# Kernel tuning notes

Hardware: AMD Instinct MI355X
Metric: run time of the kernel (lower is better)

## Reference

```python
import jax, jax.numpy as jnp
import numpy as np

ATT_RANGE = 10
R_FACTOR = 2
NHEAD = 8

def softsign(x):
    return x / (1.0 + jnp.abs(x))

def layer_norm(x, g, b, eps=1e-5):
    mu = jnp.mean(x, axis=-1, keepdims=True)
    var = jnp.var(x, axis=-1, keepdims=True)
    return (x - mu) / jnp.sqrt(var + eps) * g + b

def _forward(input_enc, input_dec, spkr_vec, speed, enc_w, enc_b, spkr_w, conv_w, speed_att_w,
             attproj_w, attproj_b, spd1_w, spd1_b, spd2_w, spd2_b, pre1_w, pre1_b, pre2_w, pre2_b,
             lstm_wih0, lstm_whh0, lstm_bih0, lstm_bhh0, lstm_wih1, lstm_whh1, lstm_bih1, lstm_bhh1,
             outl1_w, outl1_b, tr_inproj_w, tr_inproj_b, tr_out_w, tr_out_b, tr_ln1_g, tr_ln1_b,
             tr_ff1_w, tr_ff1_b, tr_ff2_w, tr_ff2_b, tr_ln2_g, tr_ln2_b, outl2_w, outl2_b, lengths_enc):
    N, T, ENC = input_enc.shape
    # first-step attention state: one-hot at t=0 (null_state branch)
    aw0 = jnp.zeros((N, T), input_enc.dtype).at[:, 0].set(1.0)
    # attention biases (null_bias branch)
    att_bias_enc = softsign(input_enc @ enc_w.T + enc_b)          # (N,T,ATT)
    att_bias_spkr = softsign(spkr_vec @ spkr_w.T)                  # (N,1,ATT)
    in_att_speed = (speed[:, None] @ speed_att_w.T)[:, None, :]    # (N,1,ATT)
    # location conv over previous attention: Conv1d(1, ATT, 31, pad 15, no bias)
    prev = jax.lax.conv_general_dilated(aw0[:, None, :], conv_w, (1,), [(15, 15)],
                                        dimension_numbers=('NCH', 'OIH', 'NCH'))  # (N,ATT,T)
    in_att_prev = prev.transpose(0, 2, 1)                          # (N,T,ATT)
    # hidden is None on first step -> in_att_dec = 0
    e = att_bias_enc + att_bias_spkr + in_att_prev + in_att_speed
    logit = jnp.tanh(e) @ attproj_w.T + attproj_b                  # (N,T,1)
    # windowed mask around argmax of previous attention (torch.no_grad)
    m = jnp.argmax(aw0, axis=1)                                    # (N,)
    t = jnp.arange(T)
    lm1 = lengths_enc - 1
    mask = ((t[None, :] >= (m - ATT_RANGE + 1)[:, None]) &
            (t[None, :] <= (m + ATT_RANGE - 1)[:, None]) &
            (t[None, :] <= lm1[:, None])).astype(logit.dtype)[..., None]
    w = jnp.exp(logit - jnp.max(logit, axis=1, keepdims=True)) * jax.lax.stop_gradient(mask)
    w = w / jnp.maximum(jnp.sum(jnp.abs(w), axis=1, keepdims=True), 1e-12)  # F.normalize p=1 dim=1
    # speed projection added to encoder features (eval mode: dropout off)
    sp = jnp.tanh(jax.nn.relu(speed[:, None] @ spd1_w.T + spd1_b) @ spd2_w.T + spd2_b)  # (N,ENC)
    enc2 = input_enc + sp[:, None, :]
    context = jnp.einsum('nt,ntc->nc', w[..., 0], enc2)[:, None, :]  # (N,1,ENC)
    # prenet on cat(input_dec, spkr)
    pin = jnp.concatenate([input_dec, spkr_vec[:, 0, :]], axis=-1)
    pre = jax.nn.relu(jax.nn.relu(pin @ pre1_w.T + pre1_b) @ pre2_w.T + pre2_b)[:, None, :]
    in_lstm = jnp.concatenate([pre, context, spkr_vec], axis=2)      # (N,1,DEC+ENC+SPK)
    # 2-layer LSTM, single timestep, zero initial state (h0=c0=0 -> Whh*h0 = 0)
    def lstm_step(x, wih, bih, bhh):
        g = x @ wih.T + bih + bhh
        i, f, gg, o = jnp.split(g, 4, axis=-1)
        c = jax.nn.sigmoid(i) * jnp.tanh(gg)
        return jax.nn.sigmoid(o) * jnp.tanh(c)
    h1 = lstm_step(in_lstm[:, 0, :], lstm_wih0, lstm_bih0, lstm_bhh0)
    h2 = lstm_step(h1, lstm_wih1, lstm_bih1, lstm_bhh1)
    out_lstm = h2[:, None, :]                                        # (N,1,4*DEC)
    # debug==14: cat(out_lstm, in_lstm) then seq-first for transformer
    x = jnp.concatenate([out_lstm, in_lstm], axis=2).transpose(1, 0, 2)  # (1,N,3136)
    x = x @ outl1_w.T + outl1_b                                      # (1,N,DEC)
    D = x.shape[-1]
    dh = D // NHEAD
    for l in range(tr_inproj_w.shape[0]):
        qkv = x @ tr_inproj_w[l].T + tr_inproj_b[l]
        q, k, v = jnp.split(qkv, 3, axis=-1)
        S, Nn, _ = q.shape
        qh = q.reshape(S, Nn, NHEAD, dh)
        kh = k.reshape(S, Nn, NHEAD, dh)
        vh = v.reshape(S, Nn, NHEAD, dh)
        a = jnp.einsum('snhd,tnhd->nhst', qh, kh) / jnp.sqrt(jnp.asarray(dh, x.dtype))
        a = jax.nn.softmax(a, axis=-1)
        att = jnp.einsum('nhst,tnhd->snhd', a, vh).reshape(S, Nn, D)
        att = att @ tr_out_w[l].T + tr_out_b[l]
        x = layer_norm(x + att, tr_ln1_g[l], tr_ln1_b[l])
        ff = jax.nn.relu(x @ tr_ff1_w[l].T + tr_ff1_b[l]) @ tr_ff2_w[l].T + tr_ff2_b[l]
        x = layer_norm(x + ff, tr_ln2_g[l], tr_ln2_b[l])
    out = (x @ outl2_w.T + outl2_b).transpose(1, 0, 2).reshape(N, R_FACTOR, -1)  # (N,2,80)
    return out, context

def setup_inputs():
    key = jax.random.key(0)
    ks = iter(jax.random.split(key, 64))
    def nrm(shape, s=0.05):
        return jax.random.normal(next(ks), shape, jnp.float32) * s
    N, T, ENC, ATT, DEC, OUT, SPK, L, FF = 32, 2048, 512, 256, 512, 80, 64, 2, 1024
    return dict(
        input_enc=nrm((N, T, ENC), 1.0),
        input_dec=nrm((N, OUT), 1.0),
        spkr_vec=nrm((N, 1, SPK), 1.0),
        speed=jax.random.uniform(next(ks), (N,), jnp.float32, 0.5, 1.5),
        lengths_enc=jnp.full((N,), T, dtype=jnp.int32),
        enc_w=nrm((ATT, ENC)), enc_b=nrm((ATT,)),
        spkr_w=nrm((ATT, SPK)),
        conv_w=nrm((ATT, 1, 31)),
        speed_att_w=nrm((ATT, 1)),
        attproj_w=nrm((1, ATT)), attproj_b=nrm((1,)),
        spd1_w=nrm((DEC, 1)), spd1_b=nrm((DEC,)), spd2_w=nrm((ENC, DEC)), spd2_b=nrm((ENC,)),
        pre1_w=nrm((2 * DEC, OUT + SPK)), pre1_b=nrm((2 * DEC,)),
        pre2_w=nrm((DEC, 2 * DEC)), pre2_b=nrm((DEC,)),
        lstm_wih0=nrm((16 * DEC, ENC + DEC + SPK)), lstm_whh0=nrm((16 * DEC, 4 * DEC)),
        lstm_bih0=nrm((16 * DEC,)), lstm_bhh0=nrm((16 * DEC,)),
        lstm_wih1=nrm((16 * DEC, 4 * DEC)), lstm_whh1=nrm((16 * DEC, 4 * DEC)),
        lstm_bih1=nrm((16 * DEC,)), lstm_bhh1=nrm((16 * DEC,)),
        outl1_w=nrm((DEC, ENC + DEC + SPK + 4 * DEC)), outl1_b=nrm((DEC,)),
        tr_inproj_w=nrm((L, 3 * DEC, DEC)), tr_inproj_b=nrm((L, 3 * DEC)),
        tr_out_w=nrm((L, DEC, DEC)), tr_out_b=nrm((L, DEC)),
        tr_ln1_g=jnp.ones((L, DEC)), tr_ln1_b=jnp.zeros((L, DEC)),
        tr_ff1_w=nrm((L, FF, DEC)), tr_ff1_b=nrm((L, FF)),
        tr_ff2_w=nrm((L, DEC, FF)), tr_ff2_b=nrm((L, DEC)),
        tr_ln2_g=jnp.ones((L, DEC)), tr_ln2_b=jnp.zeros((L, DEC)),
        outl2_w=nrm((R_FACTOR * OUT, DEC)), outl2_b=nrm((R_FACTOR * OUT,)),
    )

def reference(input_enc, input_dec, spkr_vec, speed, lengths_enc, enc_w, enc_b, spkr_w, conv_w,
              speed_att_w, attproj_w, attproj_b, spd1_w, spd1_b, spd2_w, spd2_b, pre1_w, pre1_b,
              pre2_w, pre2_b, lstm_wih0, lstm_whh0, lstm_bih0, lstm_bhh0, lstm_wih1, lstm_whh1,
              lstm_bih1, lstm_bhh1, outl1_w, outl1_b, tr_inproj_w, tr_inproj_b, tr_out_w, tr_out_b,
              tr_ln1_g, tr_ln1_b, tr_ff1_w, tr_ff1_b, tr_ff2_w, tr_ff2_b, tr_ln2_g, tr_ln2_b,
              outl2_w, outl2_b):
    return _forward(input_enc, input_dec, spkr_vec, speed, enc_w, enc_b, spkr_w, conv_w, speed_att_w,
                    attproj_w, attproj_b, spd1_w, spd1_b, spd2_w, spd2_b, pre1_w, pre1_b, pre2_w, pre2_b,
                    lstm_wih0, lstm_whh0, lstm_bih0, lstm_bhh0, lstm_wih1, lstm_whh1, lstm_bih1, lstm_bhh1,
                    outl1_w, outl1_b, tr_inproj_w, tr_inproj_b, tr_out_w, tr_out_b, tr_ln1_g, tr_ln1_b,
                    tr_ff1_w, tr_ff1_b, tr_ff2_w, tr_ff2_b, tr_ln2_g, tr_ln2_b, outl2_w, outl2_b, lengths_enc)
```

## Files before the change

### kernel.cpp

```cpp
#include <hip/hip_runtime.h>

typedef unsigned short u16;
typedef unsigned int u32;

__device__ __forceinline__ float bf2f(u16 u){ return __uint_as_float(((u32)u) << 16); }
__device__ __forceinline__ u16 f2bf(float f){
  u32 u = __float_as_uint(f);
  u32 r = u + 0x7fffu + ((u >> 16) & 1u);
  return (u16)(r >> 16);
}
__device__ __forceinline__ float lo2f(u32 u){ return __uint_as_float(u << 16); }
__device__ __forceinline__ float hi2f(u32 u){ return __uint_as_float(u & 0xffff0000u); }
__device__ __forceinline__ float uif(u32 u){ return __uint_as_float(u); }
__device__ __forceinline__ float sigf(float x){ return 1.0f / (1.0f + expf(-x)); }
__device__ __forceinline__ float wave_sum(float v){
  v += __shfl_xor(v, 1);  v += __shfl_xor(v, 2);  v += __shfl_xor(v, 4);
  v += __shfl_xor(v, 8);  v += __shfl_xor(v, 16); v += __shfl_xor(v, 32);
  return v;
}

template<int F32> __device__ __forceinline__ float IG(const void* p, size_t i){
  if constexpr (F32) return ((const float*)p)[i];
  else return bf2f(((const u16*)p)[i]);
}
template<int F32> __device__ __forceinline__ void OW(void* p, size_t i, float v){
  if constexpr (F32) ((float*)p)[i] = v;
  else ((u16*)p)[i] = f2bf(v);
}

__global__ void k_detect(const void* speed, int* flag)
{
  if (threadIdx.x == 0 && blockIdx.x == 0) {
    const u16* s = (const u16*)speed;
    int cnt = 0;
    #pragma unroll
    for (int i = 0; i < 8; ++i) {
      u16 v = s[2 * i];
      cnt += (v >= 0x3F00 && v <= 0x3FC0) ? 1 : 0;
    }
    flag[0] = (cnt >= 6) ? 0 : 1;
  }
}

template<int F32>
__global__ __launch_bounds__(256) void k_init(
    const int* __restrict__ flag,
    const void* __restrict__ dec, const void* __restrict__ spkr, const void* __restrict__ speed,
    const void* __restrict__ spd1_w, const void* __restrict__ spd1_b,
    float* __restrict__ pin, float* __restrict__ hspd, float* __restrict__ spkr_rn)
{
  if (flag[0] != F32) return;
  int idx = blockIdx.x * 256 + threadIdx.x;
  if (idx < 144 * 32) {
    int k = idx >> 5, n = idx & 31;
    float v = (k < 80) ? IG<F32>(dec, n * 80 + k) : IG<F32>(spkr, n * 64 + (k - 80));
    pin[idx] = v;
  } else if (idx < 144 * 32 + 512 * 32) {
    int j = idx - 144 * 32; int d = j >> 5, n = j & 31;
    float v = IG<F32>(speed, n) * IG<F32>(spd1_w, d) + IG<F32>(spd1_b, d);
    hspd[j] = fmaxf(v, 0.0f);
  } else if (idx < 144 * 32 + 512 * 32 + 64 * 32) {
    int j = idx - (144 * 32 + 512 * 32); int s = j >> 5, n = j & 31;
    spkr_rn[j] = IG<F32>(spkr, n * 64 + s);
  }
}

__device__ __forceinline__ float piece_fetch(int gk, int pn,
    const float* __restrict__ xa, int Ka, const float* __restrict__ xb, int Kb,
    const float* __restrict__ xc, int Kc, const float* __restrict__ xd)
{
  if (gk < Ka) return xa[(size_t)gk * 32 + pn];
  gk -= Ka;
  if (gk < Kb) return xb[(size_t)gk * 32 + pn];
  gk -= Kb;
  if (gk < Kc) return xc[(size_t)gk * 32 + pn];
  gk -= Kc;
  return xd[(size_t)gk * 32 + pn];
}

template<int F32>
__global__ __launch_bounds__(256) void k_gemv32(
    const int* __restrict__ flag,
    const float* __restrict__ xa, int Ka,
    const float* __restrict__ xb, int Kb,
    const float* __restrict__ xc, int Kc,
    const float* __restrict__ xd,
    const void* __restrict__ W,
    const void* __restrict__ bias1,
    const void* __restrict__ bias2,
    float* __restrict__ out,
    int K, int rowmap, int act)
{
  if (flag[0] != F32) return;
  __shared__ u32 xbuf[256][33];
  const int KCHE = F32 ? 256 : 512;
  int tid = threadIdx.x;
  int n = tid & 31;
  int rl = tid >> 5;
  int r = blockIdx.x * 8 + rl;
  int wr = r;
  if (rowmap && r >= 2048) wr = r + 2048;
  float acc = 0.0f;
  float acc1 = 0.0f, acc2 = 0.0f, acc3 = 0.0f;

  for (int k0 = 0; k0 < K; k0 += KCHE) {
    int kc = K - k0; if (kc > KCHE) kc = KCHE;
    if constexpr (F32) {
      for (int p = tid; p < kc * 32; p += 256) {
        int pn = p & 31, kk = p >> 5;
        xbuf[kk][pn] = __float_as_uint(piece_fetch(k0 + kk, pn, xa, Ka, xb, Kb, xc, Kc, xd));
      }
    } else {
      int pairs = kc >> 1;
      for (int p = tid; p < pairs * 32; p += 256) {
        int pn = p & 31, kk2 = p >> 5;
        int gk = k0 + 2 * kk2;
        float v0 = piece_fetch(gk,     pn, xa, Ka, xb, Kb, xc, Kc, xd);
        float v1 = piece_fetch(gk + 1, pn, xa, Ka, xb, Kb, xc, Kc, xd);
        xbuf[kk2][pn] = ((u32)f2bf(v1) << 16) | (u32)f2bf(v0);
      }
    }
    __syncthreads();
    if constexpr (F32) {
      const float4* wq = reinterpret_cast<const float4*>((const float*)W + (size_t)wr * (size_t)K + k0);
      for (int kk = 0; kk < kc; kk += 8) {
        float4 w0 = wq[(kk >> 2)];
        float4 w1 = wq[(kk >> 2) + 1];
        acc = fmaf(uif(xbuf[kk + 0][n]), w0.x, acc);
        acc = fmaf(uif(xbuf[kk + 1][n]), w0.y, acc);
        acc = fmaf(uif(xbuf[kk + 2][n]), w0.z, acc);
        acc = fmaf(uif(xbuf[kk + 3][n]), w0.w, acc);
        acc = fmaf(uif(xbuf[kk + 4][n]), w1.x, acc);
        acc = fmaf(uif(xbuf[kk + 5][n]), w1.y, acc);
        acc = fmaf(uif(xbuf[kk + 6][n]), w1.z, acc);
        acc = fmaf(uif(xbuf[kk + 7][n]), w1.w, acc);
      }
    } else {
      int pairs = kc >> 1;
      const uint4* wq = reinterpret_cast<const uint4*>((const u16*)W + (size_t)wr * (size_t)K + k0);
      int kk2 = 0;
      for (; kk2 + 16 <= pairs; kk2 += 16) {
        int q = kk2 >> 2;
        uint4 w0 = wq[q], w1 = wq[q + 1], w2 = wq[q + 2], w3 = wq[q + 3];
        u32 xw;
        xw = xbuf[kk2 +  0][n]; acc  = fmaf(lo2f(xw), lo2f(w0.x), acc ); acc  = fmaf(hi2f(xw), hi2f(w0.x), acc );
        xw = xbuf[kk2 +  1][n]; acc  = fmaf(lo2f(xw), lo2f(w0.y), acc ); acc  = fmaf(hi2f(xw), hi2f(w0.y), acc );
        xw = xbuf[kk2 +  2][n]; acc  = fmaf(lo2f(xw), lo2f(w0.z), acc ); acc  = fmaf(hi2f(xw), hi2f(w0.z), acc );
        xw = xbuf[kk2 +  3][n]; acc  = fmaf(lo2f(xw), lo2f(w0.w), acc ); acc  = fmaf(hi2f(xw), hi2f(w0.w), acc );
        xw = xbuf[kk2 +  4][n]; acc1 = fmaf(lo2f(xw), lo2f(w1.x), acc1); acc1 = fmaf(hi2f(xw), hi2f(w1.x), acc1);
        xw = xbuf[kk2 +  5][n]; acc1 = fmaf(lo2f(xw), lo2f(w1.y), acc1); acc1 = fmaf(hi2f(xw), hi2f(w1.y), acc1);
        xw = xbuf[kk2 +  6][n]; acc1 = fmaf(lo2f(xw), lo2f(w1.z), acc1); acc1 = fmaf(hi2f(xw), hi2f(w1.z), acc1);
        xw = xbuf[kk2 +  7][n]; acc1 = fmaf(lo2f(xw), lo2f(w1.w), acc1); acc1 = fmaf(hi2f(xw), hi2f(w1.w), acc1);
        xw = xbuf[kk2 +  8][n]; acc2 = fmaf(lo2f(xw), lo2f(w2.x), acc2); acc2 = fmaf(hi2f(xw), hi2f(w2.x), acc2);
        xw = xbuf[kk2 +  9][n]; acc2 = fmaf(lo2f(xw), lo2f(w2.y), acc2); acc2 = fmaf(hi2f(xw), hi2f(w2.y), acc2);
        xw = xbuf[kk2 + 10][n]; acc2 = fmaf(lo2f(xw), lo2f(w2.z), acc2); acc2 = fmaf(hi2f(xw), hi2f(w2.z), acc2);
        xw = xbuf[kk2 + 11][n]; acc2 = fmaf(lo2f(xw), lo2f(w2.w), acc2); acc2 = fmaf(hi2f(xw), hi2f(w2.w), acc2);
        xw = xbuf[kk2 + 12][n]; acc3 = fmaf(lo2f(xw), lo2f(w3.x), acc3); acc3 = fmaf(hi2f(xw), hi2f(w3.x), acc3);
        xw = xbuf[kk2 + 13][n]; acc3 = fmaf(lo2f(xw), lo2f(w3.y), acc3); acc3 = fmaf(hi2f(xw), hi2f(w3.y), acc3);
        xw = xbuf[kk2 + 14][n]; acc3 = fmaf(lo2f(xw), lo2f(w3.z), acc3); acc3 = fmaf(hi2f(xw), hi2f(w3.z), acc3);
        xw = xbuf[kk2 + 15][n]; acc3 = fmaf(lo2f(xw), lo2f(w3.w), acc3); acc3 = fmaf(hi2f(xw), hi2f(w3.w), acc3);
      }
      for (; kk2 < pairs; kk2 += 4) {
        uint4 wv = wq[kk2 >> 2];
        u32 xw;
        xw = xbuf[kk2 + 0][n]; acc = fmaf(lo2f(xw), lo2f(wv.x), acc); acc = fmaf(hi2f(xw), hi2f(wv.x), acc);
        xw = xbuf[kk2 + 1][n]; acc = fmaf(lo2f(xw), lo2f(wv.y), acc); acc = fmaf(hi2f(xw), hi2f(wv.y), acc);
        xw = xbuf[kk2 + 2][n]; acc = fmaf(lo2f(xw), lo2f(wv.z), acc); acc = fmaf(hi2f(xw), hi2f(wv.z), acc);
        xw = xbuf[kk2 + 3][n]; acc = fmaf(lo2f(xw), lo2f(wv.w), acc); acc = fmaf(hi2f(xw), hi2f(wv.w), acc);
      }
    }
    __syncthreads();
  }
  acc = (acc + acc1) + (acc2 + acc3);
  if (bias1) acc += IG<F32>(bias1, wr);
  if (bias2) acc += IG<F32>(bias2, wr);
  if (act == 1) acc = fmaxf(acc, 0.0f);
  else if (act == 2) acc = tanhf(acc);
  out[(size_t)r * 32 + n] = acc;
}

template<int F32>
__global__ __launch_bounds__(256) void k_att_logit(
    const int* __restrict__ flag,
    const void* __restrict__ enc, const void* __restrict__ spkr, const void* __restrict__ speed,
    const void* __restrict__ enc_w, const void* __restrict__ enc_b, const void* __restrict__ spkr_w,
    const void* __restrict__ conv_w, const void* __restrict__ speed_att_w,
    const void* __restrict__ attproj_w, const void* __restrict__ attproj_b,
    float* __restrict__ logits)
{
  if (flag[0] != F32) return;
  int t = blockIdx.x;
  int n = blockIdx.y;
  int tid = threadIdx.x;
  __shared__ float encL[512];
  __shared__ float spkL[64];
  __shared__ float red[4];
  size_t ebase = ((size_t)n * 2048 + (size_t)t) * 512;
  encL[tid]       = IG<F32>(enc, ebase + tid);
  encL[tid + 256] = IG<F32>(enc, ebase + tid + 256);
  if (tid < 64) spkL[tid] = IG<F32>(spkr, n * 64 + tid);
  __syncthreads();

  int a = tid;
  float ss = 0.0f, d = 0.0f;
  if constexpr (F32) {
    const float4* sw = reinterpret_cast<const float4*>((const float*)spkr_w + (size_t)a * 64);
    #pragma unroll
    for (int i = 0; i < 16; ++i) {
      float4 wv = sw[i]; int c0 = i * 4;
      ss = fmaf(spkL[c0 + 0], wv.x, ss); ss = fmaf(spkL[c0 + 1], wv.y, ss);
      ss = fmaf(spkL[c0 + 2], wv.z, ss); ss = fmaf(spkL[c0 + 3], wv.w, ss);
    }
    const float4* ew = reinterpret_cast<const float4*>((const float*)enc_w + (size_t)a * 512);
    #pragma unroll 8
    for (int i = 0; i < 128; ++i) {
      float4 wv = ew[i]; int c0 = i * 4;
      d = fmaf(encL[c0 + 0], wv.x, d); d = fmaf(encL[c0 + 1], wv.y, d);
      d = fmaf(encL[c0 + 2], wv.z, d); d = fmaf(encL[c0 + 3], wv.w, d);
    }
  } else {
    const uint4* sw = reinterpret_cast<const uint4*>((const u16*)spkr_w + (size_t)a * 64);
    #pragma unroll
    for (int i = 0; i < 8; ++i) {
      uint4 wv = sw[i]; int c0 = i * 8;
      ss = fmaf(spkL[c0 + 0], lo2f(wv.x), ss); ss = fmaf(spkL[c0 + 1], hi2f(wv.x), ss);
      ss = fmaf(spkL[c0 + 2], lo2f(wv.y), ss); ss = fmaf(spkL[c0 + 3], hi2f(wv.y), ss);
      ss = fmaf(spkL[c0 + 4], lo2f(wv.z), ss); ss = fmaf(spkL[c0 + 5], hi2f(wv.z), ss);
      ss = fmaf(spkL[c0 + 6], lo2f(wv.w), ss); ss = fmaf(spkL[c0 + 7], hi2f(wv.w), ss);
    }
    const uint4* ew = reinterpret_cast<const uint4*>((const u16*)enc_w + (size_t)a * 512);
    #pragma unroll 8
    for (int i = 0; i < 64; ++i) {
      uint4 wv = ew[i]; int c0 = i * 8;
      d = fmaf(encL[c0 + 0], lo2f(wv.x), d); d = fmaf(encL[c0 + 1], hi2f(wv.x), d);
      d = fmaf(encL[c0 + 2], lo2f(wv.y), d); d = fmaf(encL[c0 + 3], hi2f(wv.y), d);
      d = fmaf(encL[c0 + 4], lo2f(wv.z), d); d = fmaf(encL[c0 + 5], hi2f(wv.z), d);
      d = fmaf(encL[c0 + 6], lo2f(wv.w), d); d = fmaf(encL[c0 + 7], hi2f(wv.w), d);
    }
  }
  float bspk = ss / (1.0f + fabsf(ss));
  float spd = IG<F32>(speed, n) * IG<F32>(speed_att_w, a);
  float arg = d + IG<F32>(enc_b, a);
  float be = arg / (1.0f + fabsf(arg));
  float e = be + bspk + IG<F32>(conv_w, a * 31 + (15 - t)) + spd;
  float p = tanhf(e) * IG<F32>(attproj_w, a);

  float s = wave_sum(p);
  int wid = tid >> 6;
  if ((tid & 63) == 0) red[wid] = s;
  __syncthreads();
  if (tid == 0) {
    logits[n * 16 + t] = red[0] + red[1] + red[2] + red[3] + IG<F32>(attproj_b, 0);
  }
}

template<int F32>
__global__ __launch_bounds__(256) void k_ctx2(
    const int* __restrict__ flag,
    const void* __restrict__ enc, const int* __restrict__ lengths,
    const float* __restrict__ logits, const float* __restrict__ sp,
    float* __restrict__ ctx, void* __restrict__ out)
{
  if (flag[0] != F32) return;
  int n = blockIdx.x, tid = threadIdx.x;
  __shared__ float wL[10];
  if (tid == 0) {
    int lm1 = lengths[n] - 1;
    float lf[10]; float m = -3.0e38f;
    #pragma unroll
    for (int t = 0; t < 10; ++t) { lf[t] = logits[n * 16 + t]; if (t <= lm1 && lf[t] > m) m = lf[t]; }
    float s = 0.0f, w[10];
    #pragma unroll
    for (int t = 0; t < 10; ++t) { w[t] = (t <= lm1) ? expf(lf[t] - m) : 0.0f; s += w[t]; }
    float dnm = fmaxf(s, 1e-12f);
    #pragma unroll
    for (int t = 0; t < 10; ++t) wL[t] = w[t] / dnm;
  }
  __syncthreads();
  for (int c = tid; c < 512; c += 256) {
    float spv = sp[(size_t)c * 32 + n];
    float acc = 0.0f;
    size_t base = (size_t)n * 2048 * 512 + c;
    #pragma unroll
    for (int t = 0; t < 10; ++t) acc += wL[t] * (IG<F32>(enc, base + (size_t)t * 512) + spv);
    ctx[(size_t)c * 32 + n] = acc;
    OW<F32>(out, 5120 + n * 512 + c, acc);
  }
}

__global__ __launch_bounds__(256) void k_act(const float* __restrict__ g, float* __restrict__ h)
{
  int f = blockIdx.x * 256 + threadIdx.x;
  int j = f >> 5, n = f & 31;
  float gi = g[(size_t)j * 32 + n];
  float gg = g[(size_t)(2048 + j) * 32 + n];
  float go = g[(size_t)(4096 + j) * 32 + n];
  float c = sigf(gi) * tanhf(gg);
  h[f] = sigf(go) * tanhf(c);
}

template<int F32>
__global__ __launch_bounds__(512) void k_attln(
    const int* __restrict__ flag,
    float* __restrict__ x,
    const void* __restrict__ Wv, const void* __restrict__ bv,
    const void* __restrict__ Wo, const void* __restrict__ bo,
    const void* __restrict__ lg, const void* __restrict__ lb)
{
  if (flag[0] != F32) return;
  int n = blockIdx.x, tid = threadIdx.x;
  __shared__ __align__(16) float xL[512];
  __shared__ __align__(16) float vL[512];
  __shared__ float red[18];
  xL[tid] = x[(size_t)tid * 32 + n];
  __syncthreads();

  const float4* x4 = reinterpret_cast<const float4*>(xL);
  float acc = 0.0f;
  if constexpr (F32) {
    const float4* wq = reinterpret_cast<const float4*>((const float*)Wv + (size_t)tid * 512);
    #pragma unroll 8
    for (int i = 0; i < 128; ++i) {
      float4 wv = wq[i]; float4 a0 = x4[i];
      acc = fmaf(a0.x, wv.x, acc); acc = fmaf(a0.y, wv.y, acc);
      acc = fmaf(a0.z, wv.z, acc); acc = fmaf(a0.w, wv.w, acc);
    }
  } else {
    const uint4* wq = reinterpret_cast<const uint4*>((const u16*)Wv + (size_t)tid * 512);
    #pragma unroll 8
    for (int i = 0; i < 64; ++i) {
      uint4 wv = wq[i];
      float4 a0 = x4[i * 2], a1 = x4[i * 2 + 1];
      acc = fmaf(a0.x, lo2f(wv.x), acc); acc = fmaf(a0.y, hi2f(wv.x), acc);
      acc = fmaf(a0.z, lo2f(wv.y), acc); acc = fmaf(a0.w, hi2f(wv.y), acc);
      acc = fmaf(a1.x, lo2f(wv.z), acc); acc = fmaf(a1.y, hi2f(wv.z), acc);
      acc = fmaf(a1.z, lo2f(wv.w), acc); acc = fmaf(a1.w, hi2f(wv.w), acc);
    }
  }
  vL[tid] = acc + IG<F32>(bv, tid);
  __syncthreads();

  const float4* v4 = reinterpret_cast<const float4*>(vL);
  float a2 = 0.0f;
  if constexpr (F32) {
    const float4* wq = reinterpret_cast<const float4*>((const float*)Wo + (size_t)tid * 512);
    #pragma unroll 8
    for (int i = 0; i < 128; ++i) {
      float4 wv = wq[i]; float4 a0 = v4[i];
      a2 = fmaf(a0.x, wv.x, a2); a2 = fmaf(a0.y, wv.y, a2);
      a2 = fmaf(a0.z, wv.z, a2); a2 = fmaf(a0.w, wv.w, a2);
    }
  } else {
    const uint4* wq = reinterpret_cast<const uint4*>((const u16*)Wo + (size_t)tid * 512);
    #pragma unroll 8
    for (int i = 0; i < 64; ++i) {
      uint4 wv = wq[i];
      float4 a0 = v4[i * 2], a1 = v4[i * 2 + 1];
      a2 = fmaf(a0.x, lo2f(wv.x), a2); a2 = fmaf(a0.y, hi2f(wv.x), a2);
      a2 = fmaf(a0.z, lo2f(wv.y), a2); a2 = fmaf(a0.w, hi2f(wv.y), a2);
      a2 = fmaf(a1.x, lo2f(wv.z), a2); a2 = fmaf(a1.y, hi2f(wv.z), a2);
      a2 = fmaf(a1.z, lo2f(wv.w), a2); a2 = fmaf(a1.w, hi2f(wv.w), a2);
    }
  }
  float y = xL[tid] + a2 + IG<F32>(bo, tid);

  float s1 = wave_sum(y), s2 = wave_sum(y * y);
  int wid = tid >> 6;
  if ((tid & 63) == 0) { red[wid] = s1; red[8 + wid] = s2; }
  __syncthreads();
  if (tid == 0) {
    float t1 = 0, t2 = 0;
    for (int i = 0; i < 8; ++i) { t1 += red[i]; t2 += red[8 + i]; }
    float mu = t1 * (1.0f / 512.0f);
    float var = t2 * (1.0f / 512.0f) - mu * mu;
    red[16] = mu; red[17] = rsqrtf(var + 1e-5f);
  }
  __syncthreads();
  float mu = red[16], rs = red[17];
  x[(size_t)tid * 32 + n] = (y - mu) * rs * IG<F32>(lg, tid) + IG<F32>(lb, tid);
}

template<int F32>
__global__ __launch_bounds__(512) void k_ff(
    const int* __restrict__ flag,
    float* __restrict__ x,
    const void* __restrict__ W1, const void* __restrict__ b1,
    const void* __restrict__ W2, const void* __restrict__ b2,
    const void* __restrict__ lg, const void* __restrict__ lb)
{
  if (flag[0] != F32) return;
  int n = blockIdx.x, tid = threadIdx.x;
  __shared__ __align__(16) float xL[512];
  __shared__ __align__(16) float hL[1024];
  __shared__ float red[18];
  xL[tid] = x[(size_t)tid * 32 + n];
  __syncthreads();

  const float4* x4 = reinterpret_cast<const float4*>(xL);
  for (int dd = tid; dd < 1024; dd += 512) {
    float acc = 0.0f;
    if constexpr (F32) {
      const float4* wq = reinterpret_cast<const float4*>((const float*)W1 + (size_t)dd * 512);
      #pragma unroll 8
      for (int i = 0; i < 128; ++i) {
        float4 wv = wq[i]; float4 a0 = x4[i];
        acc = fmaf(a0.x, wv.x, acc); acc = fmaf(a0.y, wv.y, acc);
        acc = fmaf(a0.z, wv.z, acc); acc = fmaf(a0.w, wv.w, acc);
      }
    } else {
      const uint4* wq = reinterpret_cast<const uint4*>((const u16*)W1 + (size_t)dd * 512);
      #pragma unroll 8
      for (int i = 0; i < 64; ++i) {
        uint4 wv = wq[i];
        float4 a0 = x4[i * 2], a1 = x4[i * 2 + 1];
        acc = fmaf(a0.x, lo2f(wv.x), acc); acc = fmaf(a0.y, hi2f(wv.x), acc);
        acc = fmaf(a0.z, lo2f(wv.y), acc); acc = fmaf(a0.w, hi2f(wv.y), acc);
        acc = fmaf(a1.x, lo2f(wv.z), acc); acc = fmaf(a1.y, hi2f(wv.z), acc);
        acc = fmaf(a1.z, lo2f(wv.w), acc); acc = fmaf(a1.w, hi2f(wv.w), acc);
      }
    }
    hL[dd] = fmaxf(acc + IG<F32>(b1, dd), 0.0f);
  }
  __syncthreads();

  const float4* h4 = reinterpret_cast<const float4*>(hL);
  float a2 = 0.0f;
  if constexpr (F32) {
    const float4* wq = reinterpret_cast<const float4*>((const float*)W2 + (size_t)tid * 1024);
    #pragma unroll 8
    for (int i = 0; i < 256; ++i) {
      float4 wv = wq[i]; float4 a0 = h4[i];
      a2 = fmaf(a0.x, wv.x, a2); a2 = fmaf(a0.y, wv.y, a2);
      a2 = fmaf(a0.z, wv.z, a2); a2 = fmaf(a0.w, wv.w, a2);
    }
  } else {
    const uint4* wq = reinterpret_cast<const uint4*>((const u16*)W2 + (size_t)tid * 1024);
    #pragma unroll 8
    for (int i = 0; i < 128; ++i) {
      uint4 wv = wq[i];
      float4 a0 = h4[i * 2], a1 = h4[i * 2 + 1];
      a2 = fmaf(a0.x, lo2f(wv.x), a2); a2 = fmaf(a0.y, hi2f(wv.x), a2);
      a2 = fmaf(a0.z, lo2f(wv.y), a2); a2 = fmaf(a0.w, hi2f(wv.y), a2);
      a2 = fmaf(a1.x, lo2f(wv.z), a2); a2 = fmaf(a1.y, hi2f(wv.z), a2);
      a2 = fmaf(a1.z, lo2f(wv.w), a2); a2 = fmaf(a1.w, hi2f(wv.w), a2);
    }
  }
  float y = xL[tid] + a2 + IG<F32>(b2, tid);

  float s1 = wave_sum(y), s2 = wave_sum(y * y);
  int wid = tid >> 6;
  if ((tid & 63) == 0) { red[wid] = s1; red[8 + wid] = s2; }
  __syncthreads();
  if (tid == 0) {
    float t1 = 0, t2 = 0;
    for (int i = 0; i < 8; ++i) { t1 += red[i]; t2 += red[8 + i]; }
    float mu = t1 * (1.0f / 512.0f);
    float var = t2 * (1.0f / 512.0f) - mu * mu;
    red[16] = mu; red[17] = rsqrtf(var + 1e-5f);
  }
  __syncthreads();
  float mu = red[16], rs = red[17];
  x[(size_t)tid * 32 + n] = (y - mu) * rs * IG<F32>(lg, tid) + IG<F32>(lb, tid);
}

template<int F32>
__global__ __launch_bounds__(256) void k_out2(
    const int* __restrict__ flag,
    const float* __restrict__ x, const void* __restrict__ W, const void* __restrict__ bias,
    void* __restrict__ out)
{
  if (flag[0] != F32) return;
  int n = blockIdx.x, tid = threadIdx.x;
  __shared__ __align__(16) float xL[512];
  xL[tid]       = x[(size_t)tid * 32 + n];
  xL[tid + 256] = x[(size_t)(tid + 256) * 32 + n];
  __syncthreads();
  if (tid < 160) {
    const float4* x4 = reinterpret_cast<const float4*>(xL);
    float acc = 0.0f;
    if constexpr (F32) {
      const float4* wq = reinterpret_cast<const float4*>((const float*)W + (size_t)tid * 512);
      #pragma unroll 8
      for (int i = 0; i < 128; ++i) {
        float4 wv = wq[i]; float4 a0 = x4[i];
        acc = fmaf(a0.x, wv.x, acc); acc = fmaf(a0.y, wv.y, acc);
        acc = fmaf(a0.z, wv.z, acc); acc = fmaf(a0.w, wv.w, acc);
      }
    } else {
      const uint4* wq = reinterpret_cast<const uint4*>((const u16*)W + (size_t)tid * 512);
      #pragma unroll 8
      for (int i = 0; i < 64; ++i) {
        uint4 wv = wq[i];
        float4 a0 = x4[i * 2], a1 = x4[i * 2 + 1];
        acc = fmaf(a0.x, lo2f(wv.x), acc); acc = fmaf(a0.y, hi2f(wv.x), acc);
        acc = fmaf(a0.z, lo2f(wv.y), acc); acc = fmaf(a0.w, hi2f(wv.y), acc);
        acc = fmaf(a1.x, lo2f(wv.z), acc); acc = fmaf(a1.y, hi2f(wv.z), acc);
        acc = fmaf(a1.z, lo2f(wv.w), acc); acc = fmaf(a1.w, hi2f(wv.w), acc);
      }
    }
    OW<F32>(out, n * 160 + tid, acc + IG<F32>(bias, tid));
  }
}

template<int F32>
static void run_pipeline(void* const* d_in, void* d_out, float* wsf, int* flag,
                         hipStream_t stream)
{
  const void* IN_ENC   = d_in[0];
  const void* IN_DEC   = d_in[1];
  const void* SPKR     = d_in[2];
  const void* SPEED    = d_in[3];
  const int*  LENGTHS  = (const int*)d_in[4];
  const void* ENC_W    = d_in[5];
  const void* ENC_B    = d_in[6];
  const void* SPKR_W   = d_in[7];
  const void* CONV_W   = d_in[8];
  const void* SPEEDA_W = d_in[9];
  const void* ATTP_W   = d_in[10];
  const void* ATTP_B   = d_in[11];
  const void* SPD1_W   = d_in[12];
  const void* SPD1_B   = d_in[13];
  const void* SPD2_W   = d_in[14];
  const void* SPD2_B   = d_in[15];
  const void* PRE1_W   = d_in[16];
  const void* PRE1_B   = d_in[17];
  const void* PRE2_W   = d_in[18];
  const void* PRE2_B   = d_in[19];
  const void* WIH0     = d_in[20];
  const void* BIH0     = d_in[22];
  const void* BHH0     = d_in[23];
  const void* WIH1     = d_in[24];
  const void* BIH1     = d_in[26];
  const void* BHH1     = d_in[27];
  const void* OUTL1_W  = d_in[28];
  const void* OUTL1_B  = d_in[29];
  const void* INPROJ_W = d_in[30];
  const void* INPROJ_B = d_in[31];
  const void* TOUT_W   = d_in[32];
  const void* TOUT_B   = d_in[33];
  const void* LN1_G    = d_in[34];
  const void* LN1_B    = d_in[35];
  const void* FF1_W    = d_in[36];
  const void* FF1_B    = d_in[37];
  const void* FF2_W    = d_in[38];
  const void* FF2_B    = d_in[39];
  const void* LN2_G    = d_in[40];
  const void* LN2_B    = d_in[41];
  const void* OUTL2_W  = d_in[42];
  const void* OUTL2_B  = d_in[43];

  float* pin     = wsf + 0;
  float* hspd    = wsf + 4608;
  float* spkr_rn = wsf + 20992;
  float* sp      = wsf + 23040;
  float* logits  = wsf + 39424;
  float* ctx     = wsf + 39936;
  float* prehid  = wsf + 56320;
  float* pre     = wsf + 89088;
  float* g0      = wsf + 105472;
  float* h1      = wsf + 302080;
  float* g1      = g0;
  float* h2      = wsf + 367616;
  float* xs      = wsf + 433152;

  k_init<F32><<<90, 256, 0, stream>>>(flag, IN_DEC, SPKR, SPEED, SPD1_W, SPD1_B,
                                      pin, hspd, spkr_rn);
  k_gemv32<F32><<<64, 256, 0, stream>>>(flag, hspd, 512, hspd, 0, hspd, 0, hspd,
                                        SPD2_W, SPD2_B, nullptr, sp, 512, 0, 2);
  k_att_logit<F32><<<dim3(10, 32), 256, 0, stream>>>(flag, IN_ENC, SPKR, SPEED,
                                        ENC_W, ENC_B, SPKR_W, CONV_W, SPEEDA_W,
                                        ATTP_W, ATTP_B, logits);
  k_ctx2<F32><<<32, 256, 0, stream>>>(flag, IN_ENC, LENGTHS, logits, sp, ctx, d_out);
  k_gemv32<F32><<<128, 256, 0, stream>>>(flag, pin, 144, pin, 0, pin, 0, pin,
                                         PRE1_W, PRE1_B, nullptr, prehid, 144, 0, 1);
  k_gemv32<F32><<<64, 256, 0, stream>>>(flag, prehid, 1024, prehid, 0, prehid, 0, prehid,
                                        PRE2_W, PRE2_B, nullptr, pre, 1024, 0, 1);
  k_gemv32<F32><<<768, 256, 0, stream>>>(flag, pre, 512, ctx, 512, spkr_rn, 64, pre,
                                         WIH0, BIH0, BHH0, g0, 1088, 1, 0);
  k_act<<<256, 256, 0, stream>>>(g0, h1);
  k_gemv32<F32><<<768, 256, 0, stream>>>(flag, h1, 2048, h1, 0, h1, 0, h1,
                                         WIH1, BIH1, BHH1, g1, 2048, 1, 0);
  k_act<<<256, 256, 0, stream>>>(g1, h2);
  k_gemv32<F32><<<64, 256, 0, stream>>>(flag, h2, 2048, pre, 512, ctx, 512, spkr_rn,
                                        OUTL1_W, OUTL1_B, nullptr, xs, 3136, 0, 0);

  for (int l = 0; l < 2; ++l) {
    size_t e = F32 ? 1 : 1;
    const char* Wv = (const char*)INPROJ_W; const char* bv = (const char*)INPROJ_B;
    const char* Wo = (const char*)TOUT_W;   const char* bo = (const char*)TOUT_B;
    const char* W1 = (const char*)FF1_W;    const char* W2 = (const char*)FF2_W;
    int esz = F32 ? 4 : 2;
    k_attln<F32><<<32, 512, 0, stream>>>(flag, xs,
        Wv + ((size_t)l * 786432 + 524288) * esz,
        bv + ((size_t)l * 1536 + 1024) * esz,
        Wo + ((size_t)l * 262144) * esz,
        bo + ((size_t)l * 512) * esz,
        (const char*)LN1_G + (size_t)l * 512 * esz,
        (const char*)LN1_B + (size_t)l * 512 * esz);
    k_ff<F32><<<32, 512, 0, stream>>>(flag, xs,
        W1 + ((size_t)l * 524288) * esz,
        (const char*)FF1_B + (size_t)l * 1024 * esz,
        W2 + ((size_t)l * 524288) * esz,
        (const char*)FF2_B + (size_t)l * 512 * esz,
        (const char*)LN2_G + (size_t)l * 512 * esz,
        (const char*)LN2_B + (size_t)l * 512 * esz);
    (void)e;
  }

  k_out2<F32><<<32, 256, 0, stream>>>(flag, xs, OUTL2_W, OUTL2_B, d_out);
}

extern "C" void kernel_launch(void* const* d_in, const int* in_sizes, int n_in,
                              void* d_out, int out_size, void* d_ws, size_t ws_size,
                              hipStream_t stream)
{
  float* wsf = (float*)d_ws;
  int* flag = (int*)(wsf + 458752);

  k_detect<<<1, 64, 0, stream>>>(d_in[3], flag);

  run_pipeline<0>(d_in, d_out, wsf, flag, stream);
  run_pipeline<1>(d_in, d_out, wsf, flag, stream);
}
```

Measured before the change: 772.6 us.

## Split LSTM gate GEMVs along K into two launches and halve the shared-memory staging tile

Each LSTM gate GEMV is split into two sequential launches, each covering half of the K dimension. Partial results are written to separate workspace buffers and summed in a new activation kernel, k_act2. The shared-memory x staging buffer is halved, which may raise occupancy. The trade-off is extra launches, extra partial-sum traffic and more sync rounds per K range. The split path runs only when the workspace is large enough.

```diff
diff --git a/kernel.cpp b/kernel.cpp
--- a/kernel.cpp
+++ b/kernel.cpp
@@ -89,11 +89,11 @@
     const void* __restrict__ bias1,
     const void* __restrict__ bias2,
     float* __restrict__ out,
-    int K, int rowmap, int act)
+    int K, int kbase, int Kfull, int rowmap, int act)
 {
   if (flag[0] != F32) return;
-  __shared__ u32 xbuf[256][33];
-  const int KCHE = F32 ? 256 : 512;
+  __shared__ u32 xbuf[128][33];
+  const int KCHE = F32 ? 128 : 256;
   int tid = threadIdx.x;
   int n = tid & 31;
   int rl = tid >> 5;
@@ -108,13 +108,13 @@
     if constexpr (F32) {
       for (int p = tid; p < kc * 32; p += 256) {
         int pn = p & 31, kk = p >> 5;
-        xbuf[kk][pn] = __float_as_uint(piece_fetch(k0 + kk, pn, xa, Ka, xb, Kb, xc, Kc, xd));
+        xbuf[kk][pn] = __float_as_uint(piece_fetch(kbase + k0 + kk, pn, xa, Ka, xb, Kb, xc, Kc, xd));
       }
     } else {
       int pairs = kc >> 1;
       for (int p = tid; p < pairs * 32; p += 256) {
         int pn = p & 31, kk2 = p >> 5;
-        int gk = k0 + 2 * kk2;
+        int gk = kbase + k0 + 2 * kk2;
         float v0 = piece_fetch(gk,     pn, xa, Ka, xb, Kb, xc, Kc, xd);
         float v1 = piece_fetch(gk + 1, pn, xa, Ka, xb, Kb, xc, Kc, xd);
         xbuf[kk2][pn] = ((u32)f2bf(v1) << 16) | (u32)f2bf(v0);
@@ -122,7 +122,7 @@
     }
     __syncthreads();
     if constexpr (F32) {
-      const float4* wq = reinterpret_cast<const float4*>((const float*)W + (size_t)wr * (size_t)K + k0);
+      const float4* wq = reinterpret_cast<const float4*>((const float*)W + (size_t)wr * (size_t)Kfull + kbase + k0);
       for (int kk = 0; kk < kc; kk += 8) {
         float4 w0 = wq[(kk >> 2)];
         float4 w1 = wq[(kk >> 2) + 1];
@@ -137,7 +137,7 @@
       }
     } else {
       int pairs = kc >> 1;
-      const uint4* wq = reinterpret_cast<const uint4*>((const u16*)W + (size_t)wr * (size_t)K + k0);
+      const uint4* wq = reinterpret_cast<const uint4*>((const u16*)W + (size_t)wr * (size_t)Kfull + kbase + k0);
       int kk2 = 0;
       for (; kk2 + 16 <= pairs; kk2 += 16) {
         int q = kk2 >> 2;
@@ -299,6 +299,18 @@
   h[f] = sigf(go) * tanhf(c);
 }
 
+__global__ __launch_bounds__(256) void k_act2(
+    const float* __restrict__ ga, const float* __restrict__ gb, float* __restrict__ h)
+{
+  int f = blockIdx.x * 256 + threadIdx.x;
+  int j = f >> 5, n = f & 31;
+  float gi = ga[(size_t)j * 32 + n]          + gb[(size_t)j * 32 + n];
+  float gg = ga[(size_t)(2048 + j) * 32 + n] + gb[(size_t)(2048 + j) * 32 + n];
+  float go = ga[(size_t)(4096 + j) * 32 + n] + gb[(size_t)(4096 + j) * 32 + n];
+  float c = sigf(gi) * tanhf(gg);
+  h[f] = sigf(go) * tanhf(c);
+}
+
 template<int F32>
 __global__ __launch_bounds__(512) void k_attln(
     const int* __restrict__ flag,
@@ -504,7 +516,7 @@
 
 template<int F32>
 static void run_pipeline(void* const* d_in, void* d_out, float* wsf, int* flag,
-                         hipStream_t stream)
+                         int do_split, float* gpartB, hipStream_t stream)
 {
   const void* IN_ENC   = d_in[0];
   const void* IN_DEC   = d_in[1];
@@ -566,26 +578,40 @@
   k_init<F32><<<90, 256, 0, stream>>>(flag, IN_DEC, SPKR, SPEED, SPD1_W, SPD1_B,
                                       pin, hspd, spkr_rn);
   k_gemv32<F32><<<64, 256, 0, stream>>>(flag, hspd, 512, hspd, 0, hspd, 0, hspd,
-                                        SPD2_W, SPD2_B, nullptr, sp, 512, 0, 2);
+                                        SPD2_W, SPD2_B, nullptr, sp, 512, 0, 512, 0, 2);
   k_att_logit<F32><<<dim3(10, 32), 256, 0, stream>>>(flag, IN_ENC, SPKR, SPEED,
                                         ENC_W, ENC_B, SPKR_W, CONV_W, SPEEDA_W,
                                         ATTP_W, ATTP_B, logits);
   k_ctx2<F32><<<32, 256, 0, stream>>>(flag, IN_ENC, LENGTHS, logits, sp, ctx, d_out);
   k_gemv32<F32><<<128, 256, 0, stream>>>(flag, pin, 144, pin, 0, pin, 0, pin,
-                                         PRE1_W, PRE1_B, nullptr, prehid, 144, 0, 1);
+                                         PRE1_W, PRE1_B, nullptr, prehid, 144, 0, 144, 0, 1);
   k_gemv32<F32><<<64, 256, 0, stream>>>(flag, prehid, 1024, prehid, 0, prehid, 0, prehid,
-                                        PRE2_W, PRE2_B, nullptr, pre, 1024, 0, 1);
-  k_gemv32<F32><<<768, 256, 0, stream>>>(flag, pre, 512, ctx, 512, spkr_rn, 64, pre,
-                                         WIH0, BIH0, BHH0, g0, 1088, 1, 0);
-  k_act<<<256, 256, 0, stream>>>(g0, h1);
-  k_gemv32<F32><<<768, 256, 0, stream>>>(flag, h1, 2048, h1, 0, h1, 0, h1,
-                                         WIH1, BIH1, BHH1, g1, 2048, 1, 0);
-  k_act<<<256, 256, 0, stream>>>(g1, h2);
+                                        PRE2_W, PRE2_B, nullptr, pre, 1024, 0, 1024, 0, 1);
+
+  if (do_split) {
+    k_gemv32<F32><<<768, 256, 0, stream>>>(flag, pre, 512, ctx, 512, spkr_rn, 64, pre,
+                                           WIH0, nullptr, nullptr, g0, 544, 0, 1088, 1, 0);
+    k_gemv32<F32><<<768, 256, 0, stream>>>(flag, pre, 512, ctx, 512, spkr_rn, 64, pre,
+                                           WIH0, BIH0, BHH0, gpartB, 544, 544, 1088, 1, 0);
+    k_act2<<<256, 256, 0, stream>>>(g0, gpartB, h1);
+    k_gemv32<F32><<<768, 256, 0, stream>>>(flag, h1, 2048, h1, 0, h1, 0, h1,
+                                           WIH1, nullptr, nullptr, g1, 1024, 0, 2048, 1, 0);
+    k_gemv32<F32><<<768, 256, 0, stream>>>(flag, h1, 2048, h1, 0, h1, 0, h1,
+                                           WIH1, BIH1, BHH1, gpartB, 1024, 1024, 2048, 1, 0);
+    k_act2<<<256, 256, 0, stream>>>(g1, gpartB, h2);
+  } else {
+    k_gemv32<F32><<<768, 256, 0, stream>>>(flag, pre, 512, ctx, 512, spkr_rn, 64, pre,
+                                           WIH0, BIH0, BHH0, g0, 1088, 0, 1088, 1, 0);
+    k_act<<<256, 256, 0, stream>>>(g0, h1);
+    k_gemv32<F32><<<768, 256, 0, stream>>>(flag, h1, 2048, h1, 0, h1, 0, h1,
+                                           WIH1, BIH1, BHH1, g1, 2048, 0, 2048, 1, 0);
+    k_act<<<256, 256, 0, stream>>>(g1, h2);
+  }
+
   k_gemv32<F32><<<64, 256, 0, stream>>>(flag, h2, 2048, pre, 512, ctx, 512, spkr_rn,
-                                        OUTL1_W, OUTL1_B, nullptr, xs, 3136, 0, 0);
+                                        OUTL1_W, OUTL1_B, nullptr, xs, 3136, 0, 3136, 0, 0);
 
   for (int l = 0; l < 2; ++l) {
-    size_t e = F32 ? 1 : 1;
     const char* Wv = (const char*)INPROJ_W; const char* bv = (const char*)INPROJ_B;
     const char* Wo = (const char*)TOUT_W;   const char* bo = (const char*)TOUT_B;
     const char* W1 = (const char*)FF1_W;    const char* W2 = (const char*)FF2_W;
@@ -604,7 +630,6 @@
         (const char*)FF2_B + (size_t)l * 512 * esz,
         (const char*)LN2_G + (size_t)l * 512 * esz,
         (const char*)LN2_B + (size_t)l * 512 * esz);
-    (void)e;
   }
 
   k_out2<F32><<<32, 256, 0, stream>>>(flag, xs, OUTL2_W, OUTL2_B, d_out);
@@ -616,9 +641,11 @@
 {
   float* wsf = (float*)d_ws;
   int* flag = (int*)(wsf + 458752);
+  float* gpartB = wsf + 460800;
+  int do_split = (ws_size >= (size_t)(460800 + 196608) * 4) ? 1 : 0;
 
   k_detect<<<1, 64, 0, stream>>>(d_in[3], flag);
 
-  run_pipeline<0>(d_in, d_out, wsf, flag, stream);
-  run_pipeline<1>(d_in, d_out, wsf, flag, stream);
-}
+  run_pipeline<0>(d_in, d_out, wsf, flag, do_split, gpartB, stream);
+  run_pipeline<1>(d_in, d_out, wsf, flag, do_split, gpartB, stream);
+}
```

Result: no change. 784.6 us (+1.6%).
